# Optimization experiments

Hardware: AMD Instinct MI355X
Metric: run time of the kernel (lower is better)

## Reference

```python
import jax, jax.numpy as jnp
import numpy as np

LEAKY_SLOPE = 0.2  # DGL GATConv default negative_slope


def setup_inputs() -> dict:
    key = jax.random.key(0)
    ks = jax.random.split(key, 10)
    N_SRC, N_DST, E = 100000, 100000, 1600000
    H1, H0, D = 2, 2, 32          # in_h1_heads, in_h0_heads (GAT num_heads), out_dim
    IN1, IN0 = 128, 128           # in_h1_dim, in_h0_dim
    OUT_HEADS = 4
    return {
        "hier_1": jax.random.normal(ks[0], (N_SRC, H1, IN1), jnp.float32),
        "hier_0": jax.random.normal(ks[1], (N_DST, IN0), jnp.float32),
        "src_idx": jax.random.randint(ks[2], (E,), 0, N_SRC, jnp.int32),
        "dst_idx": jax.random.randint(ks[3], (E,), 0, N_DST, jnp.int32),
        "W_src": jax.random.normal(ks[4], (H0 * D, IN1), jnp.float32) * 0.05,
        "W_dst": jax.random.normal(ks[5], (H0 * D, IN0), jnp.float32) * 0.05,
        "attn_l": jax.random.normal(ks[6], (H0, D), jnp.float32) * 0.1,
        "attn_r": jax.random.normal(ks[7], (H0, D), jnp.float32) * 0.1,
        "gat_bias": jnp.zeros((H0, D), jnp.float32),
        "fc_W": jax.random.normal(ks[8], (OUT_HEADS, H1 * H0), jnp.float32),
        "fc_b": jnp.zeros((OUT_HEADS,), jnp.float32),
    }


def reference(hier_1, hier_0, src_idx, dst_idx, W_src, W_dst,
              attn_l, attn_r, gat_bias, fc_W, fc_b):
    N_src, H1, _ = hier_1.shape
    N_dst = hier_0.shape[0]
    H0, D = attn_l.shape

    # Shared GATConv projections (same weights reused across the H1 python loop
    # in the original -> vectorize over the H1 axis).
    feat_src = jnp.einsum('nhi,oi->nho', hier_1, W_src).reshape(N_src, H1, H0, D)
    feat_dst = (hier_0 @ W_dst.T).reshape(N_dst, H0, D)

    el = jnp.einsum('nhkd,kd->nhk', feat_src, attn_l)   # [N_src, H1, H0]
    er = jnp.einsum('nkd,kd->nk', feat_dst, attn_r)     # [N_dst, H0]

    # Edge attention logits + softmax over incoming edges per dst node.
    e = jax.nn.leaky_relu(el[src_idx] + er[dst_idx][:, None, :], LEAKY_SLOPE)  # [E,H1,H0]
    emax = jax.ops.segment_max(e, dst_idx, num_segments=N_dst)
    emax = jnp.where(jnp.isfinite(emax), emax, 0.0)     # zero-in-degree safety
    ee = jnp.exp(e - emax[dst_idx])
    denom = jax.ops.segment_sum(ee, dst_idx, num_segments=N_dst)
    alpha = ee / denom[dst_idx]                          # [E, H1, H0]

    # Aggregate messages: sum_e alpha * feat_src[src].
    msg = alpha[..., None] * feat_src[src_idx]           # [E, H1, H0, D]
    out = jax.ops.segment_sum(msg, dst_idx, num_segments=N_dst)  # [N_dst,H1,H0,D]
    out = out + gat_bias[None, None]                     # GATConv bias (per call)

    # cat over H1 (H1-major), transpose, softmax-normalized linear head mixing.
    res = out.reshape(N_dst, H1 * H0, D)
    res = jnp.swapaxes(res, 1, 2)                        # [N_dst, D, H1*H0]
    W = jax.nn.softmax(fc_W, axis=1)                     # normWeight: softmax(dim=1)
    res = res @ W.T + fc_b                               # [N_dst, D, out_heads]
    return jnp.swapaxes(res, 1, 2)                       # [N_dst, out_heads, D]
```

## Files before the change

kernel.cpp:

```cpp
#include <hip/hip_runtime.h>
#include <hip/hip_bf16.h>

typedef __attribute__((ext_vector_type(8))) short short8_t;
typedef __attribute__((ext_vector_type(4))) float float4v;

__device__ __forceinline__ float lrelu(float x) { return x > 0.f ? x : 0.2f * x; }
__device__ __forceinline__ float blo(unsigned u) { return __uint_as_float(u << 16); }
__device__ __forceinline__ float bhi(unsigned u) { return __uint_as_float(u & 0xffff0000u); }

__device__ __forceinline__ short8_t mk8(unsigned a, unsigned b, unsigned c, unsigned d) {
    union { unsigned u[4]; short8_t s; } x;
    x.u[0] = a; x.u[1] = b; x.u[2] = c; x.u[3] = d;
    return x.s;
}

__device__ __forceinline__ void split8(const float4& f0, const float4& f1,
                                       short8_t& hi8, short8_t& lo8) {
    float xs[8] = {f0.x, f0.y, f0.z, f0.w, f1.x, f1.y, f1.z, f1.w};
    unsigned h[4], l4[4];
#pragma unroll
    for (int p = 0; p < 4; ++p) {
        unsigned b0 = __float_as_uint(xs[2 * p]);
        unsigned b1 = __float_as_uint(xs[2 * p + 1]);
        unsigned h0b = b0 & 0xffff0000u, h1b = b1 & 0xffff0000u;
        h[p] = (h0b >> 16) | h1b;
        float l0 = xs[2 * p] - __uint_as_float(h0b);
        float l1 = xs[2 * p + 1] - __uint_as_float(h1b);
        l4[p] = (__float_as_uint(l0) >> 16) | (__float_as_uint(l1) & 0xffff0000u);
    }
    hi8 = mk8(h[0], h[1], h[2], h[3]);
    lo8 = mk8(l4[0], l4[1], l4[2], l4[3]);
}

__global__ void k_prep(const float* __restrict__ Wdst,
                       const float* __restrict__ attn_r,
                       const float* __restrict__ fcW,
                       const float* __restrict__ fcb,
                       const float* __restrict__ Wsrc,
                       float* __restrict__ w_er, float* __restrict__ Wn,
                       float* __restrict__ fb,
                       unsigned short* __restrict__ Wb_hi,
                       unsigned short* __restrict__ Wb_lo) {
    int t = threadIdx.x;
#pragma unroll
    for (int j = 0; j < 32; ++j) {
        int i = t + j * 256;
        float x = Wsrc[i];
        unsigned hb = __float_as_uint(x) & 0xffff0000u;
        float lf = x - __uint_as_float(hb);
        Wb_hi[i] = (unsigned short)(hb >> 16);
        Wb_lo[i] = (unsigned short)(__float_as_uint(lf) >> 16);
    }
    {
        int h0 = t >> 7, i = t & 127;
        float s = 0.f;
        for (int d = 0; d < 32; ++d)
            s += attn_r[h0 * 32 + d] * Wdst[(size_t)(h0 * 32 + d) * 128 + i];
        w_er[t] = s;
    }
    if (t < 16) {
        int oh = t >> 2, k = t & 3;
        float w[4], m = -1e30f;
        for (int j = 0; j < 4; ++j) {
            w[j] = fcW[oh * 4 + j];
            m = fmaxf(m, w[j]);
        }
        float s = 0.f;
        for (int j = 0; j < 4; ++j) s += __expf(w[j] - m);
        Wn[t] = __expf(w[k] - m) / s;
    }
    if (t < 4) fb[t] = fcb[t];
}

__global__ void k_hist(const int* __restrict__ dst, int* __restrict__ deg, int E) {
    int e = blockIdx.x * blockDim.x + threadIdx.x;
    if (e < E) atomicAdd(&deg[dst[e]], 1);
}

__global__ void k_alloc(const int* __restrict__ deg, int* __restrict__ off,
                        int* __restrict__ cursor, int* __restrict__ counter,
                        int N) {
    int d = blockIdx.x * blockDim.x + threadIdx.x;
    int lane = threadIdx.x & 63;
    int v = (d < N) ? deg[d] : 0;
    int inc = v;
#pragma unroll
    for (int m = 1; m < 64; m <<= 1) {
        int u = __shfl_up(inc, m, 64);
        if (lane >= m) inc += u;
    }
    int excl = inc - v;
    int base = 0;
    if (lane == 63) base = atomicAdd(counter, inc);
    base = __shfl(base, 63, 64);
    if (d < N) {
        off[d] = base + excl;
        cursor[d] = base + excl;
    }
}

__global__ __launch_bounds__(256) void k_featA(
        const float* __restrict__ hier1, const float* __restrict__ hier0,
        const unsigned short* __restrict__ Wb_hi,
        const unsigned short* __restrict__ Wb_lo,
        const float* __restrict__ attn_l, const float* __restrict__ w_er,
        const int* __restrict__ srcIdx, const int* __restrict__ dstIdx,
        int* __restrict__ cursor, int* __restrict__ ssrc,
        __hip_bfloat16* __restrict__ featb, float* __restrict__ el,
        float* __restrict__ er,
        int nrows, int Ndst, int E, int ntiles, int ntilesT) {
    int t = threadIdx.x;
    int w = t >> 6, lane = t & 63;
    int lr = lane & 15;
    int lg = lane >> 4;

    int e = blockIdx.x * 256 + t;
    bool hasE = e < E;
    int es = 0, ed = 0;
    if (hasE) { es = srcIdx[e]; ed = dstIdx[e]; }

    int tile = blockIdx.x * 4 + w;
    bool isFeat = tile < ntiles;
    bool isEr = (tile >= ntiles) && (tile < ntilesT);

    float4 areg[8];
    if (isFeat || isEr) {
        const float* hrow;
        if (isFeat) {
            int row_l = tile * 16 + lr;
            if (row_l >= nrows) row_l = nrows - 1;
            hrow = hier1 + (size_t)row_l * 128 + lg * 8;
        } else {
            int node = (tile - ntiles) * 16 + lr;
            if (node >= Ndst) node = Ndst - 1;
            hrow = hier0 + (size_t)node * 128 + lg * 8;
        }
#pragma unroll
        for (int kc = 0; kc < 4; ++kc) {
            areg[2 * kc]     = *reinterpret_cast<const float4*>(hrow + kc * 32);
            areg[2 * kc + 1] = *reinterpret_cast<const float4*>(hrow + kc * 32 + 4);
        }
    }

    if (hasE) {
        int pos = atomicAdd(&cursor[ed], 1);
        ssrc[pos] = es;
    }

    if (!(isFeat || isEr)) return;

    short8_t a_hi[4], a_lo[4];
#pragma unroll
    for (int kc = 0; kc < 4; ++kc)
        split8(areg[2 * kc], areg[2 * kc + 1], a_hi[kc], a_lo[kc]);

    if (isFeat) {
        int m0 = tile * 16;
        float4v acc[4];
#pragma unroll
        for (int n = 0; n < 4; ++n) acc[n] = (float4v){0.f, 0.f, 0.f, 0.f};
#pragma unroll
        for (int n = 0; n < 4; ++n) {
            const unsigned short* bh = Wb_hi + (size_t)(n * 16 + lr) * 128 + lg * 8;
            const unsigned short* bl = Wb_lo + (size_t)(n * 16 + lr) * 128 + lg * 8;
#pragma unroll
            for (int kc = 0; kc < 4; ++kc) {
                short8_t Bh = *reinterpret_cast<const short8_t*>(bh + kc * 32);
                short8_t Bl = *reinterpret_cast<const short8_t*>(bl + kc * 32);
                acc[n] = __builtin_amdgcn_mfma_f32_16x16x32_bf16(a_lo[kc], Bh, acc[n], 0, 0, 0);
                acc[n] = __builtin_amdgcn_mfma_f32_16x16x32_bf16(a_hi[kc], Bl, acc[n], 0, 0, 0);
                acc[n] = __builtin_amdgcn_mfma_f32_16x16x32_bf16(a_hi[kc], Bh, acc[n], 0, 0, 0);
            }
        }

        float pe0[4] = {0.f, 0.f, 0.f, 0.f};
        float pe1[4] = {0.f, 0.f, 0.f, 0.f};
#pragma unroll
        for (int n = 0; n < 4; ++n) {
            float al = attn_l[n * 16 + lr];
#pragma unroll
            for (int r = 0; r < 4; ++r) {
                int row = m0 + lg * 4 + r;
                float v = acc[n][r];
                if (row < nrows)
                    featb[((size_t)(row >> 1)) * 128 + (row & 1) * 64 + n * 16 + lr] =
                        __float2bfloat16(v);
                if (n < 2) pe0[r] += v * al; else pe1[r] += v * al;
            }
        }
#pragma unroll
        for (int m = 1; m <= 8; m <<= 1) {
#pragma unroll
            for (int r = 0; r < 4; ++r) {
                pe0[r] += __shfl_xor(pe0[r], m, 64);
                pe1[r] += __shfl_xor(pe1[r], m, 64);
            }
        }
        if (lr < 2) {
#pragma unroll
            for (int r = 0; r < 4; ++r) {
                int row = m0 + lg * 4 + r;
                float ev = lr ? pe1[r] : pe0[r];
                if (row < nrows) el[row * 2 + lr] = ev;
            }
        }
    } else {
        int m0 = (tile - ntiles) * 16;
        short8_t Bh[4], Bl[4];
#pragma unroll
        for (int kc = 0; kc < 4; ++kc) {
            Bh[kc] = mk8(0, 0, 0, 0);
            Bl[kc] = mk8(0, 0, 0, 0);
        }
        if (lr < 2) {
#pragma unroll
            for (int kc = 0; kc < 4; ++kc) {
                float4 f0 = *reinterpret_cast<const float4*>(w_er + lr * 128 + kc * 32 + lg * 8);
                float4 f1 = *reinterpret_cast<const float4*>(w_er + lr * 128 + kc * 32 + lg * 8 + 4);
                split8(f0, f1, Bh[kc], Bl[kc]);
            }
        }
        float4v acc = (float4v){0.f, 0.f, 0.f, 0.f};
#pragma unroll
        for (int kc = 0; kc < 4; ++kc) {
            acc = __builtin_amdgcn_mfma_f32_16x16x32_bf16(a_lo[kc], Bh[kc], acc, 0, 0, 0);
            acc = __builtin_amdgcn_mfma_f32_16x16x32_bf16(a_hi[kc], Bl[kc], acc, 0, 0, 0);
            acc = __builtin_amdgcn_mfma_f32_16x16x32_bf16(a_hi[kc], Bh[kc], acc, 0, 0, 0);
        }
        if (lr < 2) {
#pragma unroll
            for (int r = 0; r < 4; ++r) {
                int nn = m0 + lg * 4 + r;
                if (nn < Ndst) er[nn * 2 + lr] = acc[r];
            }
        }
    }
}

__global__ __launch_bounds__(256) void k_gather(
        const int* __restrict__ ssrc, const int* __restrict__ off,
        const int* __restrict__ deg,
        const float* __restrict__ el, const float* __restrict__ er,
        const uint4* __restrict__ feat4,
        const float* __restrict__ bias,
        const float* __restrict__ Wn, const float* __restrict__ fb,
        float* __restrict__ out, int Ndst, int E) {
    __shared__ float g[4][128];
    int t = threadIdx.x;
    int wv = t >> 6, lane = t & 63;
    int d = blockIdx.x * 4 + wv;
    bool valid = d < Ndst;

    int q = lane >> 3;
    int c = lane & 7;
    int k = c >> 1;
    float erk = valid ? er[d * 2 + (k & 1)] : 0.f;
    int start = valid ? off[d] : 0;
    int n = valid ? deg[d] : 0;

    float a[16];
#pragma unroll
    for (int j = 0; j < 16; ++j) a[j] = 0.f;
    float den = 0.f;

    int base = start + q;
    int sA = ssrc[base < E ? base : 0];
    int sB = ssrc[(base + 8) < E ? (base + 8) : 0];
    uint4 fA0 = feat4[(size_t)sA * 16 + 2 * c];
    uint4 fA1 = feat4[(size_t)sA * 16 + 2 * c + 1];
    float eA = el[sA * 4 + k];

    for (int i = 0; i < n; i += 8) {
        uint4 fB0 = feat4[(size_t)sB * 16 + 2 * c];
        uint4 fB1 = feat4[(size_t)sB * 16 + 2 * c + 1];
        float eB = el[sB * 4 + k];
        int nx = base + i + 16;
        int sC = ssrc[nx < E ? nx : 0];

        bool ve = (i + q) < n;
        float ee = ve ? __expf(lrelu(eA + erk)) : 0.f;
        den += ee;
        a[0]  = fmaf(ee, blo(fA0.x), a[0]);
        a[1]  = fmaf(ee, bhi(fA0.x), a[1]);
        a[2]  = fmaf(ee, blo(fA0.y), a[2]);
        a[3]  = fmaf(ee, bhi(fA0.y), a[3]);
        a[4]  = fmaf(ee, blo(fA0.z), a[4]);
        a[5]  = fmaf(ee, bhi(fA0.z), a[5]);
        a[6]  = fmaf(ee, blo(fA0.w), a[6]);
        a[7]  = fmaf(ee, bhi(fA0.w), a[7]);
        a[8]  = fmaf(ee, blo(fA1.x), a[8]);
        a[9]  = fmaf(ee, bhi(fA1.x), a[9]);
        a[10] = fmaf(ee, blo(fA1.y), a[10]);
        a[11] = fmaf(ee, bhi(fA1.y), a[11]);
        a[12] = fmaf(ee, blo(fA1.z), a[12]);
        a[13] = fmaf(ee, bhi(fA1.z), a[13]);
        a[14] = fmaf(ee, blo(fA1.w), a[14]);
        a[15] = fmaf(ee, bhi(fA1.w), a[15]);

        sB = sC; fA0 = fB0; fA1 = fB1; eA = eB;
    }

#pragma unroll
    for (int m = 8; m <= 32; m <<= 1) {
        den += __shfl_xor(den, m, 64);
#pragma unroll
        for (int j = 0; j < 16; ++j) a[j] += __shfl_xor(a[j], m, 64);
    }

    float inv = den > 0.f ? 1.f / den : 0.f;
    if (q == 0) {
        int h0 = k & 1;
        int db = (c & 1) * 16;
#pragma unroll
        for (int j = 0; j < 16; ++j)
            g[wv][c * 16 + j] = a[j] * inv + bias[h0 * 32 + db + j];
    }
    __syncthreads();

    if (valid) {
        int dd = (lane & 15) * 2;
        int oh = lane >> 4;
        float r0 = fb[oh], r1 = r0;
#pragma unroll
        for (int kk = 0; kk < 4; ++kk) {
            float wgt = Wn[oh * 4 + kk];
            r0 = fmaf(g[wv][kk * 32 + dd], wgt, r0);
            r1 = fmaf(g[wv][kk * 32 + dd + 1], wgt, r1);
        }
        *reinterpret_cast<float2*>(out + (size_t)d * 128 + lane * 2) =
            make_float2(r0, r1);
    }
}

extern "C" void kernel_launch(void* const* d_in, const int* in_sizes, int n_in,
                              void* d_out, int out_size, void* d_ws, size_t ws_size,
                              hipStream_t stream) {
    (void)n_in; (void)out_size; (void)ws_size;
    const float* hier1  = (const float*)d_in[0];
    const float* hier0  = (const float*)d_in[1];
    const int*   srcIdx = (const int*)d_in[2];
    const int*   dstIdx = (const int*)d_in[3];
    const float* Wsrc   = (const float*)d_in[4];
    const float* Wdst   = (const float*)d_in[5];
    const float* attn_l = (const float*)d_in[6];
    const float* attn_r = (const float*)d_in[7];
    const float* bias   = (const float*)d_in[8];
    const float* fcW    = (const float*)d_in[9];
    const float* fcb    = (const float*)d_in[10];
    float* out = (float*)d_out;

    const int Nsrc  = in_sizes[0] / 256;
    const int Ndst  = in_sizes[1] / 128;
    const int E     = in_sizes[2];
    const int nrows = Nsrc * 2;
    const int ntiles  = (nrows + 15) / 16;
    const int ntilesE = (Ndst + 15) / 16;
    const int ntilesT = ntiles + ntilesE;

    __hip_bfloat16* featb = (__hip_bfloat16*)d_ws;
    unsigned short* Wb_hi = (unsigned short*)(featb + (size_t)Nsrc * 128);
    unsigned short* Wb_lo = Wb_hi + 8192;
    float* el   = (float*)(Wb_lo + 8192);
    float* er   = el   + (size_t)nrows * 2;
    float* w_er = er   + (size_t)Ndst * 2;
    float* Wn   = w_er + 256;
    float* fb   = Wn + 16;
    int*  deg     = (int*)(fb + 4);
    int*  off     = deg + Ndst;
    int*  cursor  = off + Ndst;
    int*  counter = cursor + Ndst;
    int*  ssrc    = counter + 1;

    hipMemsetAsync(deg, 0, (size_t)Ndst * sizeof(int), stream);
    hipMemsetAsync(counter, 0, sizeof(int), stream);

    k_prep<<<1, 256, 0, stream>>>(Wdst, attn_r, fcW, fcb, Wsrc,
                                  w_er, Wn, fb, Wb_hi, Wb_lo);

    k_hist<<<(E + 255) / 256, 256, 0, stream>>>(dstIdx, deg, E);

    k_alloc<<<(Ndst + 255) / 256, 256, 0, stream>>>(deg, off, cursor, counter, Ndst);

    int blocksA = (ntilesT + 3) / 4;
    int blocksE2 = (E + 255) / 256;
    if (blocksE2 > blocksA) blocksA = blocksE2;
    k_featA<<<blocksA, 256, 0, stream>>>(hier1, hier0, Wb_hi, Wb_lo,
                                         attn_l, w_er,
                                         srcIdx, dstIdx, cursor, ssrc,
                                         featb, el, er,
                                         nrows, Ndst, E, ntiles, ntilesT);

    k_gather<<<(Ndst + 3) / 4, 256, 0, stream>>>(ssrc, off, deg, el, er,
                                                 (const uint4*)featb,
                                                 bias, Wn, fb, out, Ndst, E);
}
```

Measured before the change: 462.5 us.

## Pad atomic counters, pack per-node records, merge hist with prep, nontemporal stores

Merges the weight-prep kernel into the histogram kernel as block 0, removing one launch. Degree and cursor counters are padded to 64-byte stride so atomics on different nodes do not share cache lines. Offset, degree and the two er values are packed into one int4 record per destination, so the gather kernel needs a single load for them. It also adds nontemporal stores for ssrc and featb, changes the gather prefetch to load the second feature half one step later, and sets occupancy 8 in launch bounds. In exchange, the padded arrays make the memset and the counter footprint 16x larger.

Result: slower. 485.9 us (+5.1%).

```diff
diff --git a/kernel.cpp b/kernel.cpp
--- a/kernel.cpp
+++ b/kernel.cpp
@@ -32,57 +32,58 @@
     lo8 = mk8(l4[0], l4[1], l4[2], l4[3]);
 }
 
-__global__ void k_prep(const float* __restrict__ Wdst,
-                       const float* __restrict__ attn_r,
-                       const float* __restrict__ fcW,
-                       const float* __restrict__ fcb,
-                       const float* __restrict__ Wsrc,
-                       float* __restrict__ w_er, float* __restrict__ Wn,
-                       float* __restrict__ fb,
-                       unsigned short* __restrict__ Wb_hi,
-                       unsigned short* __restrict__ Wb_lo) {
+__global__ void k_histprep(const int* __restrict__ dst, int* __restrict__ deg_p,
+                           const float* __restrict__ Wdst,
+                           const float* __restrict__ attn_r,
+                           const float* __restrict__ fcW,
+                           const float* __restrict__ fcb,
+                           const float* __restrict__ Wsrc,
+                           float* __restrict__ w_er, float* __restrict__ Wn,
+                           float* __restrict__ fb,
+                           unsigned short* __restrict__ Wb_hi,
+                           unsigned short* __restrict__ Wb_lo, int E) {
     int t = threadIdx.x;
-#pragma unroll
-    for (int j = 0; j < 32; ++j) {
-        int i = t + j * 256;
-        float x = Wsrc[i];
-        unsigned hb = __float_as_uint(x) & 0xffff0000u;
-        float lf = x - __uint_as_float(hb);
-        Wb_hi[i] = (unsigned short)(hb >> 16);
-        Wb_lo[i] = (unsigned short)(__float_as_uint(lf) >> 16);
-    }
-    {
-        int h0 = t >> 7, i = t & 127;
-        float s = 0.f;
-        for (int d = 0; d < 32; ++d)
-            s += attn_r[h0 * 32 + d] * Wdst[(size_t)(h0 * 32 + d) * 128 + i];
-        w_er[t] = s;
-    }
-    if (t < 16) {
-        int oh = t >> 2, k = t & 3;
-        float w[4], m = -1e30f;
-        for (int j = 0; j < 4; ++j) {
-            w[j] = fcW[oh * 4 + j];
-            m = fmaxf(m, w[j]);
-        }
-        float s = 0.f;
-        for (int j = 0; j < 4; ++j) s += __expf(w[j] - m);
-        Wn[t] = __expf(w[k] - m) / s;
-    }
-    if (t < 4) fb[t] = fcb[t];
-}
-
-__global__ void k_hist(const int* __restrict__ dst, int* __restrict__ deg, int E) {
-    int e = blockIdx.x * blockDim.x + threadIdx.x;
-    if (e < E) atomicAdd(&deg[dst[e]], 1);
-}
-
-__global__ void k_alloc(const int* __restrict__ deg, int* __restrict__ off,
-                        int* __restrict__ cursor, int* __restrict__ counter,
+    if (blockIdx.x == 0) {
+#pragma unroll
+        for (int j = 0; j < 32; ++j) {
+            int i = t + j * 256;
+            float x = Wsrc[i];
+            unsigned hb = __float_as_uint(x) & 0xffff0000u;
+            float lf = x - __uint_as_float(hb);
+            Wb_hi[i] = (unsigned short)(hb >> 16);
+            Wb_lo[i] = (unsigned short)(__float_as_uint(lf) >> 16);
+        }
+        {
+            int h0 = t >> 7, i = t & 127;
+            float s = 0.f;
+            for (int d = 0; d < 32; ++d)
+                s += attn_r[h0 * 32 + d] * Wdst[(size_t)(h0 * 32 + d) * 128 + i];
+            w_er[t] = s;
+        }
+        if (t < 16) {
+            int oh = t >> 2, k = t & 3;
+            float w[4], m = -1e30f;
+            for (int j = 0; j < 4; ++j) {
+                w[j] = fcW[oh * 4 + j];
+                m = fmaxf(m, w[j]);
+            }
+            float s = 0.f;
+            for (int j = 0; j < 4; ++j) s += __expf(w[j] - m);
+            Wn[t] = __expf(w[k] - m) / s;
+        }
+        if (t < 4) fb[t] = fcb[t];
+        return;
+    }
+    int e = (blockIdx.x - 1) * 256 + t;
+    if (e < E) atomicAdd(&deg_p[(size_t)dst[e] * 16], 1);
+}
+
+__global__ void k_alloc(const int* __restrict__ deg_p, int* __restrict__ odrec,
+                        int* __restrict__ cursor_p, int* __restrict__ counter,
                         int N) {
     int d = blockIdx.x * blockDim.x + threadIdx.x;
     int lane = threadIdx.x & 63;
-    int v = (d < N) ? deg[d] : 0;
+    int v = (d < N) ? deg_p[(size_t)d * 16] : 0;
     int inc = v;
 #pragma unroll
     for (int m = 1; m < 64; m <<= 1) {
@@ -94,8 +95,9 @@
     if (lane == 63) base = atomicAdd(counter, inc);
     base = __shfl(base, 63, 64);
     if (d < N) {
-        off[d] = base + excl;
-        cursor[d] = base + excl;
+        int off = base + excl;
+        reinterpret_cast<int2*>(odrec)[(size_t)d * 2] = make_int2(off, v);
+        cursor_p[(size_t)d * 16] = off;
     }
 }
 
@@ -105,9 +107,9 @@
         const unsigned short* __restrict__ Wb_lo,
         const float* __restrict__ attn_l, const float* __restrict__ w_er,
         const int* __restrict__ srcIdx, const int* __restrict__ dstIdx,
-        int* __restrict__ cursor, int* __restrict__ ssrc,
-        __hip_bfloat16* __restrict__ featb, float* __restrict__ el,
-        float* __restrict__ er,
+        int* __restrict__ cursor_p, int* __restrict__ ssrc,
+        unsigned short* __restrict__ featb, float* __restrict__ el,
+        float* __restrict__ erbuf,
         int nrows, int Ndst, int E, int ntiles, int ntilesT) {
     int t = threadIdx.x;
     int w = t >> 6, lane = t & 63;
@@ -143,8 +145,8 @@
     }
 
     if (hasE) {
-        int pos = atomicAdd(&cursor[ed], 1);
-        ssrc[pos] = es;
+        int pos = atomicAdd(&cursor_p[(size_t)ed * 16], 1);
+        __builtin_nontemporal_store(es, &ssrc[pos]);
     }
 
     if (!(isFeat || isEr)) return;
@@ -182,9 +184,12 @@
             for (int r = 0; r < 4; ++r) {
                 int row = m0 + lg * 4 + r;
                 float v = acc[n][r];
-                if (row < nrows)
-                    featb[((size_t)(row >> 1)) * 128 + (row & 1) * 64 + n * 16 + lr] =
-                        __float2bfloat16(v);
+                if (row < nrows) {
+                    __hip_bfloat16 bv = __float2bfloat16(v);
+                    unsigned short us = *reinterpret_cast<unsigned short*>(&bv);
+                    __builtin_nontemporal_store(us,
+                        &featb[((size_t)(row >> 1)) * 128 + (row & 1) * 64 + n * 16 + lr]);
+                }
                 if (n < 2) pe0[r] += v * al; else pe1[r] += v * al;
             }
         }
@@ -231,16 +236,15 @@
 #pragma unroll
             for (int r = 0; r < 4; ++r) {
                 int nn = m0 + lg * 4 + r;
-                if (nn < Ndst) er[nn * 2 + lr] = acc[r];
-            }
-        }
-    }
-}
-
-__global__ __launch_bounds__(256) void k_gather(
-        const int* __restrict__ ssrc, const int* __restrict__ off,
-        const int* __restrict__ deg,
-        const float* __restrict__ el, const float* __restrict__ er,
+                if (nn < Ndst) erbuf[(size_t)nn * 4 + 2 + lr] = acc[r];
+            }
+        }
+    }
+}
+
+__global__ __launch_bounds__(256, 8) void k_gather(
+        const int* __restrict__ ssrc, const int4* __restrict__ odrec,
+        const float* __restrict__ el,
         const uint4* __restrict__ feat4,
         const float* __restrict__ bias,
         const float* __restrict__ Wn, const float* __restrict__ fb,
@@ -254,9 +258,10 @@
     int q = lane >> 3;
     int c = lane & 7;
     int k = c >> 1;
-    float erk = valid ? er[d * 2 + (k & 1)] : 0.f;
-    int start = valid ? off[d] : 0;
-    int n = valid ? deg[d] : 0;
+
+    int4 rec = valid ? odrec[d] : make_int4(0, 0, 0, 0);
+    int start = rec.x, n = rec.y;
+    float erk = (k & 1) ? __int_as_float(rec.w) : __int_as_float(rec.z);
 
     float a[16];
 #pragma unroll
@@ -264,18 +269,17 @@
     float den = 0.f;
 
     int base = start + q;
-    int sA = ssrc[base < E ? base : 0];
-    int sB = ssrc[(base + 8) < E ? (base + 8) : 0];
-    uint4 fA0 = feat4[(size_t)sA * 16 + 2 * c];
-    uint4 fA1 = feat4[(size_t)sA * 16 + 2 * c + 1];
-    float eA = el[sA * 4 + k];
+    int sCur = ssrc[base < E ? base : 0];
+    int sNext = ssrc[(base + 8) < E ? (base + 8) : 0];
+    uint4 fA0 = feat4[(size_t)sCur * 16 + 2 * c];
+    float eA = el[sCur * 4 + k];
 
     for (int i = 0; i < n; i += 8) {
-        uint4 fB0 = feat4[(size_t)sB * 16 + 2 * c];
-        uint4 fB1 = feat4[(size_t)sB * 16 + 2 * c + 1];
-        float eB = el[sB * 4 + k];
+        uint4 fA1 = feat4[(size_t)sCur * 16 + 2 * c + 1];
+        uint4 fB0 = feat4[(size_t)sNext * 16 + 2 * c];
+        float eB = el[sNext * 4 + k];
         int nx = base + i + 16;
-        int sC = ssrc[nx < E ? nx : 0];
+        int sFut = ssrc[nx < E ? nx : 0];
 
         bool ve = (i + q) < n;
         float ee = ve ? __expf(lrelu(eA + erk)) : 0.f;
@@ -297,7 +301,7 @@
         a[14] = fmaf(ee, blo(fA1.w), a[14]);
         a[15] = fmaf(ee, bhi(fA1.w), a[15]);
 
-        sB = sC; fA0 = fB0; fA1 = fB1; eA = eB;
+        sCur = sNext; sNext = sFut; fA0 = fB0; eA = eB;
     }
 
 #pragma unroll
@@ -357,40 +361,40 @@
     const int ntilesE = (Ndst + 15) / 16;
     const int ntilesT = ntiles + ntilesE;
 
-    __hip_bfloat16* featb = (__hip_bfloat16*)d_ws;
-    unsigned short* Wb_hi = (unsigned short*)(featb + (size_t)Nsrc * 128);
+    unsigned short* featb = (unsigned short*)d_ws;
+    unsigned short* Wb_hi = featb + (size_t)Nsrc * 128;
     unsigned short* Wb_lo = Wb_hi + 8192;
     float* el   = (float*)(Wb_lo + 8192);
-    float* er   = el   + (size_t)nrows * 2;
-    float* w_er = er   + (size_t)Ndst * 2;
+    float* w_er = el + (size_t)nrows * 2;
     float* Wn   = w_er + 256;
     float* fb   = Wn + 16;
-    int*  deg     = (int*)(fb + 4);
-    int*  off     = deg + Ndst;
-    int*  cursor  = off + Ndst;
-    int*  counter = cursor + Ndst;
-    int*  ssrc    = counter + 1;
-
-    hipMemsetAsync(deg, 0, (size_t)Ndst * sizeof(int), stream);
+    int*  deg_p    = (int*)(fb + 16);
+    int*  cursor_p = deg_p + (size_t)Ndst * 16;
+    int*  odrec    = cursor_p + (size_t)Ndst * 16;
+    int*  counter  = odrec + (size_t)Ndst * 4;
+    int*  ssrc     = counter + 4;
+
+    hipMemsetAsync(deg_p, 0, (size_t)Ndst * 16 * sizeof(int), stream);
     hipMemsetAsync(counter, 0, sizeof(int), stream);
 
-    k_prep<<<1, 256, 0, stream>>>(Wdst, attn_r, fcW, fcb, Wsrc,
-                                  w_er, Wn, fb, Wb_hi, Wb_lo);
-
-    k_hist<<<(E + 255) / 256, 256, 0, stream>>>(dstIdx, deg, E);
-
-    k_alloc<<<(Ndst + 255) / 256, 256, 0, stream>>>(deg, off, cursor, counter, Ndst);
+    int blocksH = (E + 255) / 256 + 1;
+    k_histprep<<<blocksH, 256, 0, stream>>>(dstIdx, deg_p, Wdst, attn_r,
+                                            fcW, fcb, Wsrc,
+                                            w_er, Wn, fb, Wb_hi, Wb_lo, E);
+
+    k_alloc<<<(Ndst + 255) / 256, 256, 0, stream>>>(deg_p, odrec, cursor_p,
+                                                    counter, Ndst);
 
     int blocksA = (ntilesT + 3) / 4;
     int blocksE2 = (E + 255) / 256;
     if (blocksE2 > blocksA) blocksA = blocksE2;
     k_featA<<<blocksA, 256, 0, stream>>>(hier1, hier0, Wb_hi, Wb_lo,
                                          attn_l, w_er,
-                                         srcIdx, dstIdx, cursor, ssrc,
-                                         featb, el, er,
+                                         srcIdx, dstIdx, cursor_p, ssrc,
+                                         featb, el, (float*)odrec,
                                          nrows, Ndst, E, ntiles, ntilesT);
 
-    k_gather<<<(Ndst + 3) / 4, 256, 0, stream>>>(ssrc, off, deg, el, er,
+    k_gather<<<(Ndst + 3) / 4, 256, 0, stream>>>(ssrc, (const int4*)odrec, el,
                                                  (const uint4*)featb,
                                                  bias, Wn, fb, out, Ndst, E);
 }
```
